# Kernel optimization log

Hardware: AMD Instinct MI355X
Metric: run time of the kernel (lower is better)

The kernel has to match this reference:

```python
import jax, jax.numpy as jnp
import numpy as np

EPS = 1e-08
RMAX = 8.0          # hist_range_max
BINS = 256
ALPHA = 0.02        # kalman_alpha (EMA rate)
THRESH = -2.0       # mask_threshold


def setup_inputs() -> dict:
    key = jax.random.key(0)
    B, C, L = 4, 5, 2097152
    x = jax.random.normal(key, (B, C, L), dtype=jnp.float32)
    # running histogram buffer, initialized to ones as in the module
    hist = jnp.ones((C, BINS), dtype=jnp.float32)
    # analytic reference log-pdfs over the bin grid
    grid = jnp.linspace(EPS, RMAX, BINS)
    logp_ref = jnp.stack([
        jnp.log(grid) - 0.5 * grid ** 2,                 # Rayleigh-like (A)
        -1.5 * jnp.log1p((grid / (RMAX / 2)) ** 2),      # heavy-tail (theta')
        -grid,                                            # exponential (A^2)
        -0.5 * grid ** 2,                                 # half-gaussian (AA')
        -0.5 * grid ** 2,                                 # half-gaussian (A^2 theta')
    ], axis=0) + EPS
    return {"x": x, "hist": hist, "logp_ref": logp_ref.astype(jnp.float32)}


def reference(x, hist, logp_ref):
    B, C, L = x.shape
    # NOTE: torch does x.reshape(C, -1) on a (B, C, L) tensor, i.e. a raw
    # memory reinterpretation (no permute). Replicate exactly.
    flat_abs = jnp.abs(x.reshape(C, B * L))                     # (C, B*L)
    # per-channel 99th-percentile normalization (linear interpolation, like torch)
    max_vals = jnp.maximum(
        jnp.quantile(flat_abs, 0.99, axis=-1, keepdims=True), EPS)
    normalized = flat_abs / max_vals * RMAX
    clipped = jnp.clip(normalized, 0.0, RMAX - EPS)
    idx = (clipped / RMAX * (BINS - 1)).astype(jnp.int32)       # floor (nonneg)
    idx = jnp.clip(idx, 0, BINS - 1)                            # (C, B*L)

    # histogram scatter-add per channel (vectorized over all channels)
    ch = jnp.broadcast_to(jnp.arange(C)[:, None], idx.shape)
    new_hist = jnp.zeros((C, BINS), dtype=x.dtype).at[ch, idx].add(1.0)

    # EMA update of the running histogram
    hist = (1.0 - ALPHA) * hist + ALPHA * new_hist
    smoothed = hist + EPS
    logp_obs = jnp.log(smoothed / jnp.sum(smoothed, axis=-1, keepdims=True))

    # gather per-sample log-probs and form the log-likelihood ratio
    logp_ref_s = jnp.take_along_axis(logp_ref, idx, axis=-1)   # (C, B*L)
    logp_obs_s = jnp.take_along_axis(logp_obs, idx, axis=-1)   # (C, B*L)
    Lam = (logp_ref_s - logp_obs_s).reshape(B, C, L)

    mask = jax.nn.sigmoid(-(Lam - THRESH))   # beta = 1.0
    return x * mask
```

## Files before the change

### kernel.cpp

```cpp
#include <hip/hip_runtime.h>
#include <math.h>

typedef unsigned int u32;
typedef unsigned long long u64;
typedef long long i64;

#define BINS 256
#define TBITS 0x40000000u
#define OOBBITS 0x42000000u
#define A_BASE 131072u
#define A_BINS 4096
#define B_BINS 8192
#define SLOT 2048
#define NBLK 512


__device__ __forceinline__ int bin_index_f32(float xv, float mv) {
    float r = __fdiv_rn(fabsf(xv), mv);
    r = fminf(r, 1.0f);
    return (int)__fmul_rn(r, 255.0f);
}

template<int PER>
__device__ void block_select(const u32* __restrict__ h, u32 target,
                             u32* ssum, u32* res) {
    const int t = threadIdx.x;
    u32 loc[PER];
    u32 s = 0;
    const int base = t * PER;
#pragma unroll
    for (int j = 0; j < PER; ++j) { loc[j] = h[base + j]; s += loc[j]; }
    ssum[t] = s;
    __syncthreads();
    for (int off = 1; off < 256; off <<= 1) {
        u32 add = (t >= off) ? ssum[t - off] : 0;
        __syncthreads();
        ssum[t] += add;
        __syncthreads();
    }
    u32 cum = ssum[t] - s;
#pragma unroll
    for (int j = 0; j < PER; ++j) {
        u32 cnt = loc[j];
        if (target >= cum && target < cum + cnt) { res[0] = (u32)(base + j); res[1] = target - cum; }
        cum += cnt;
    }
    __syncthreads();
}

__device__ __forceinline__ float np_lerp_f32(u32 v0bits, u32 v1bits, double gamma) {
    float v0 = __uint_as_float(v0bits);
    float v1 = __uint_as_float(v1bits);
    float dba = __fsub_rn(v1, v0);
    float q;
    if (gamma >= 0.5) q = __fsub_rn(v1, __fmul_rn(dba, (float)(1.0 - gamma)));
    else              q = __fadd_rn(v0, __fmul_rn(dba, (float)gamma));
    return fmaxf(q, 1e-8f);
}


__global__ __launch_bounds__(256) void k_pass1(const float* __restrict__ x, u32* __restrict__ cand,
                                               u32* __restrict__ oflow, i64 nper, int do_cand) {
    __shared__ u32 lbuf[SLOT];
    __shared__ u32 lcnt;
    const int c = blockIdx.y;
    if (threadIdx.x == 0) lcnt = 0;
    __syncthreads();
    const float* xc = x + (i64)c * nper;
    const i64 nv = nper >> 2;
    const float4* xv = (const float4*)xc;
    for (i64 i = (i64)blockIdx.x * 256 + threadIdx.x; i < nv; i += (i64)gridDim.x * 256) {
        float4 v = xv[i];
        u32 b;
        b = __float_as_uint(fabsf(v.x));
        if (b >= TBITS) { u32 p = atomicAdd(&lcnt, 1u); if (p < SLOT) lbuf[p] = b; }
        b = __float_as_uint(fabsf(v.y));
        if (b >= TBITS) { u32 p = atomicAdd(&lcnt, 1u); if (p < SLOT) lbuf[p] = b; }
        b = __float_as_uint(fabsf(v.z));
        if (b >= TBITS) { u32 p = atomicAdd(&lcnt, 1u); if (p < SLOT) lbuf[p] = b; }
        b = __float_as_uint(fabsf(v.w));
        if (b >= TBITS) { u32 p = atomicAdd(&lcnt, 1u); if (p < SLOT) lbuf[p] = b; }
    }
    if (blockIdx.x == 0 && threadIdx.x < (int)(nper & 3)) {
        u32 b = __float_as_uint(fabsf(xc[nv * 4 + threadIdx.x]));
        if (b >= TBITS) { u32 p = atomicAdd(&lcnt, 1u); if (p < SLOT) lbuf[p] = b; }
    }
    __syncthreads();
    if (threadIdx.x == 0 && lcnt > SLOT) {
        atomicExch(&oflow[c], 1u);
        lcnt = SLOT;
    }
    __syncthreads();
    if (do_cand) {
        const u32 cnt = lcnt;
        u32* slot = cand + ((i64)c * gridDim.x + blockIdx.x) * SLOT;
        for (u32 j = threadIdx.x; j < SLOT; j += 256)
            slot[j] = (j < cnt) ? lbuf[j] : 0u;
    }
}


__global__ __launch_bounds__(256) void k_cselA_hist(const u32* __restrict__ cand,
                                                    u32* __restrict__ gha, u32* __restrict__ goob, i64 ntot) {
    __shared__ u32 ha[A_BINS];
    __shared__ u32 loob;
    const int c = blockIdx.y;
    for (int i = threadIdx.x; i < A_BINS; i += 256) ha[i] = 0;
    if (threadIdx.x == 0) loob = 0;
    __syncthreads();
    const uint4* cd = (const uint4*)(cand + (i64)c * ntot);
    const i64 nv4 = ntot >> 2;
    for (i64 i = (i64)blockIdx.x * 256 + threadIdx.x; i < nv4; i += (i64)gridDim.x * 256) {
        uint4 v = cd[i];
        u32 b;
        b = v.x; if (b >= TBITS) { u32 bin = (b >> 13) - A_BASE; if (bin >= A_BINS) { atomicAdd(&loob, 1u); bin = A_BINS - 1; } atomicAdd(&ha[bin], 1u); }
        b = v.y; if (b >= TBITS) { u32 bin = (b >> 13) - A_BASE; if (bin >= A_BINS) { atomicAdd(&loob, 1u); bin = A_BINS - 1; } atomicAdd(&ha[bin], 1u); }
        b = v.z; if (b >= TBITS) { u32 bin = (b >> 13) - A_BASE; if (bin >= A_BINS) { atomicAdd(&loob, 1u); bin = A_BINS - 1; } atomicAdd(&ha[bin], 1u); }
        b = v.w; if (b >= TBITS) { u32 bin = (b >> 13) - A_BASE; if (bin >= A_BINS) { atomicAdd(&loob, 1u); bin = A_BINS - 1; } atomicAdd(&ha[bin], 1u); }
    }
    __syncthreads();
    for (int i = threadIdx.x; i < A_BINS; i += 256)
        if (ha[i]) atomicAdd(&gha[c * A_BINS + i], ha[i]);
    if (threadIdx.x == 0 && loob) atomicExch(&goob[c], 1u);
}

__global__ __launch_bounds__(256) void k_cselA_pick(const u32* __restrict__ gha,
                                                    const u32* __restrict__ oflow, const u32* __restrict__ goob,
                                                    u32* __restrict__ flag, u32* __restrict__ cselA, u32 needed) {
    __shared__ u32 ssum[256];
    __shared__ u32 pr[4];
    __shared__ u32 s_total;
    const int c = blockIdx.x;
    const int t = threadIdx.x;
    if (t < 4) pr[t] = 0;
    const u32* h = gha + c * A_BINS;
    u32 loc[16];
    u32 s = 0;
    const int base = t * 16;
#pragma unroll
    for (int j = 0; j < 16; ++j) { loc[j] = h[base + j]; s += loc[j]; }
    ssum[t] = s;
    __syncthreads();
    for (int off = 1; off < 256; off <<= 1) {
        u32 add = (t >= off) ? ssum[t - off] : 0;
        __syncthreads();
        ssum[t] += add;
        __syncthreads();
    }
    if (t == 255) s_total = ssum[255];
    __syncthreads();
    const u32 total = s_total;
    const u32 bad = (oflow[c] != 0) || (goob[c] != 0) || (total < needed) || (needed < 2);
    if (t == 0) flag[c] = bad;
    if (bad) return;
    const u32 t0 = total - needed;
    const u32 t1 = t0 + 1;
    u32 cum = ssum[t] - s;
#pragma unroll
    for (int j = 0; j < 16; ++j) {
        u32 cnt = loc[j];
        if (t0 >= cum && t0 < cum + cnt) { pr[0] = (u32)(base + j); pr[1] = t0 - cum; }
        if (t1 >= cum && t1 < cum + cnt) { pr[2] = (u32)(base + j); pr[3] = t1 - cum; }
        cum += cnt;
    }
    __syncthreads();
    if (t == 0) {
        cselA[c * 4 + 0] = pr[0]; cselA[c * 4 + 1] = pr[1];
        cselA[c * 4 + 2] = pr[2]; cselA[c * 4 + 3] = pr[3];
    }
}


__global__ __launch_bounds__(256) void k_cselB_hist(const u32* __restrict__ cand, const u32* __restrict__ flag,
                                                    const u32* __restrict__ cselA,
                                                    u32* __restrict__ g3a, u32* __restrict__ g3b, i64 ntot) {
    const int c = blockIdx.y;
    if (flag[c]) return;
    __shared__ u32 la[B_BINS], lb[B_BINS];
    for (int i = threadIdx.x; i < B_BINS; i += 256) { la[i] = 0; lb[i] = 0; }
    __syncthreads();
    const u32 topA0 = A_BASE + cselA[c * 4 + 0];
    const u32 topA1 = A_BASE + cselA[c * 4 + 2];
    const u32* cd = cand + (i64)c * ntot;
    for (i64 i = (i64)blockIdx.x * 256 + threadIdx.x; i < ntot; i += (i64)gridDim.x * 256) {
        u32 v = cd[i];
        if (v >= TBITS) {
            u32 tbin = v >> 13;
            if (tbin == topA0) atomicAdd(&la[v & (B_BINS - 1)], 1u);
            if (tbin == topA1) atomicAdd(&lb[v & (B_BINS - 1)], 1u);
        }
    }
    __syncthreads();
    for (int i = threadIdx.x; i < B_BINS; i += 256) {
        if (la[i]) atomicAdd(&g3a[c * B_BINS + i], la[i]);
        if (lb[i]) atomicAdd(&g3b[c * B_BINS + i], lb[i]);
    }
}

__global__ __launch_bounds__(256) void k_cselB_pick(const u32* __restrict__ g3a, const u32* __restrict__ g3b,
                                                    const u32* __restrict__ flag, const u32* __restrict__ cselA,
                                                    float* __restrict__ mv, double gamma) {
    __shared__ u32 ssum[256];
    __shared__ u32 pr[4];
    const int c = blockIdx.x;
    if (flag[c]) return;
    if (threadIdx.x < 4) pr[threadIdx.x] = 0;
    __syncthreads();
    block_select<32>(g3a + c * B_BINS, cselA[c * 4 + 1], ssum, &pr[0]);
    block_select<32>(g3b + c * B_BINS, cselA[c * 4 + 3], ssum, &pr[2]);
    if (threadIdx.x == 0) {
        u32 v0bits = ((A_BASE + cselA[c * 4 + 0]) << 13) | pr[0];
        u32 v1bits = ((A_BASE + cselA[c * 4 + 2]) << 13) | pr[2];
        mv[c] = np_lerp_f32(v0bits, v1bits, gamma);
    }
}

__global__ void k_flag_force(u32* __restrict__ flag, int C) {
    if (threadIdx.x < C) flag[threadIdx.x] = 1u;
}


__global__ __launch_bounds__(256) void k_fallback(const float* __restrict__ x, const u32* __restrict__ flag,
                                                  float* __restrict__ mv, i64 nper, u32 k0, double gamma) {
    const int c = blockIdx.x;
    if (!flag[c]) return;
    __shared__ u32 h0[2048], h1[2048];
    __shared__ u32 ssum[256];
    __shared__ u32 pr[4];
    __shared__ u32 st[4];
    const float* xc = x + (i64)c * nper;
    const i64 nv = nper >> 2;
    const int rem = (int)(nper & 3);
    const float4* xv = (const float4*)xc;
    const int t = threadIdx.x;

    for (int i = t; i < 1024; i += 256) h0[i] = 0;
    __syncthreads();
    for (i64 i = t; i < nv; i += 256) {
        float4 v = xv[i];
        atomicAdd(&h0[__float_as_uint(fabsf(v.x)) >> 21], 1u);
        atomicAdd(&h0[__float_as_uint(fabsf(v.y)) >> 21], 1u);
        atomicAdd(&h0[__float_as_uint(fabsf(v.z)) >> 21], 1u);
        atomicAdd(&h0[__float_as_uint(fabsf(v.w)) >> 21], 1u);
    }
    if (t < rem) atomicAdd(&h0[__float_as_uint(fabsf(xc[nv * 4 + t])) >> 21], 1u);
    __syncthreads();
    if (t < 4) pr[t] = 0;
    __syncthreads();
    block_select<4>(h0, k0, ssum, &pr[0]);
    block_select<4>(h0, k0 + 1, ssum, &pr[2]);
    if (t < 4) st[t] = pr[t];
    __syncthreads();

    const u32 p0 = st[0], p1 = st[2];
    for (int i = t; i < 2048; i += 256) { h0[i] = 0; h1[i] = 0; }
    __syncthreads();
    for (i64 i = t; i < nv; i += 256) {
        float4 v = xv[i];
        u32 b;
        b = __float_as_uint(fabsf(v.x));
        if ((b >> 21) == p0) atomicAdd(&h0[(b >> 10) & 2047], 1u);
        if ((b >> 21) == p1) atomicAdd(&h1[(b >> 10) & 2047], 1u);
        b = __float_as_uint(fabsf(v.y));
        if ((b >> 21) == p0) atomicAdd(&h0[(b >> 10) & 2047], 1u);
        if ((b >> 21) == p1) atomicAdd(&h1[(b >> 10) & 2047], 1u);
        b = __float_as_uint(fabsf(v.z));
        if ((b >> 21) == p0) atomicAdd(&h0[(b >> 10) & 2047], 1u);
        if ((b >> 21) == p1) atomicAdd(&h1[(b >> 10) & 2047], 1u);
        b = __float_as_uint(fabsf(v.w));
        if ((b >> 21) == p0) atomicAdd(&h0[(b >> 10) & 2047], 1u);
        if ((b >> 21) == p1) atomicAdd(&h1[(b >> 10) & 2047], 1u);
    }
    if (t < rem) {
        u32 b = __float_as_uint(fabsf(xc[nv * 4 + t]));
        if ((b >> 21) == p0) atomicAdd(&h0[(b >> 10) & 2047], 1u);
        if ((b >> 21) == p1) atomicAdd(&h1[(b >> 10) & 2047], 1u);
    }
    __syncthreads();
    if (t < 4) pr[t] = 0;
    __syncthreads();
    block_select<8>(h0, st[1], ssum, &pr[0]);
    block_select<8>(h1, st[3], ssum, &pr[2]);
    if (t == 0) { st[0] = (p0 << 11) | pr[0]; st[1] = pr[1]; st[2] = (p1 << 11) | pr[2]; st[3] = pr[3]; }
    __syncthreads();

    const u32 q0 = st[0], q1 = st[2];
    for (int i = t; i < 1024; i += 256) { h0[i] = 0; h1[i] = 0; }
    __syncthreads();
    for (i64 i = t; i < nv; i += 256) {
        float4 v = xv[i];
        u32 b;
        b = __float_as_uint(fabsf(v.x));
        if ((b >> 10) == q0) atomicAdd(&h0[b & 1023], 1u);
        if ((b >> 10) == q1) atomicAdd(&h1[b & 1023], 1u);
        b = __float_as_uint(fabsf(v.y));
        if ((b >> 10) == q0) atomicAdd(&h0[b & 1023], 1u);
        if ((b >> 10) == q1) atomicAdd(&h1[b & 1023], 1u);
        b = __float_as_uint(fabsf(v.z));
        if ((b >> 10) == q0) atomicAdd(&h0[b & 1023], 1u);
        if ((b >> 10) == q1) atomicAdd(&h1[b & 1023], 1u);
        b = __float_as_uint(fabsf(v.w));
        if ((b >> 10) == q0) atomicAdd(&h0[b & 1023], 1u);
        if ((b >> 10) == q1) atomicAdd(&h1[b & 1023], 1u);
    }
    if (t < rem) {
        u32 b = __float_as_uint(fabsf(xc[nv * 4 + t]));
        if ((b >> 10) == q0) atomicAdd(&h0[b & 1023], 1u);
        if ((b >> 10) == q1) atomicAdd(&h1[b & 1023], 1u);
    }
    __syncthreads();
    if (t < 4) pr[t] = 0;
    __syncthreads();
    block_select<4>(h0, st[1], ssum, &pr[0]);
    block_select<4>(h1, st[3], ssum, &pr[2]);
    if (t == 0) {
        u32 v0bits = (q0 << 10) | pr[0];
        u32 v1bits = (q1 << 10) | pr[2];
        mv[c] = np_lerp_f32(v0bits, v1bits, gamma);
    }
}


__global__ __launch_bounds__(256) void k_hist_idx(const float* __restrict__ x, const float* __restrict__ mv,
                                                  u32* __restrict__ h256, i64 nper) {
    __shared__ u32 lh[8][257];
    const int c = blockIdx.y;
    const float m = mv[c];
    for (int i = threadIdx.x; i < 8 * 257; i += 256) (&lh[0][0])[i] = 0;
    __syncthreads();
    const float* xc = x + (i64)c * nper;
    const i64 nv = nper >> 2;
    const int copy = threadIdx.x & 7;
    const float4* xv = (const float4*)xc;
    for (i64 i = (i64)blockIdx.x * 256 + threadIdx.x; i < nv; i += (i64)gridDim.x * 256) {
        float4 v = xv[i];
        atomicAdd(&lh[copy][bin_index_f32(v.x, m)], 1u);
        atomicAdd(&lh[copy][bin_index_f32(v.y, m)], 1u);
        atomicAdd(&lh[copy][bin_index_f32(v.z, m)], 1u);
        atomicAdd(&lh[copy][bin_index_f32(v.w, m)], 1u);
    }
    if (blockIdx.x == 0 && threadIdx.x < (int)(nper & 3)) {
        atomicAdd(&lh[copy][bin_index_f32(xc[nv * 4 + threadIdx.x], m)], 1u);
    }
    __syncthreads();
    for (int i = threadIdx.x; i < BINS; i += 256) {
        u32 s = 0;
#pragma unroll
        for (int k = 0; k < 8; ++k) s += lh[k][i];
        if (s) atomicAdd(&h256[c * BINS + i], s);
    }
}


__global__ void k_mask_table(const float* __restrict__ hist_in, const float* __restrict__ logp_ref,
                             const u32* __restrict__ h256, double* __restrict__ mask) {
    __shared__ double sm[BINS];
    __shared__ double ssum;
    const int c = blockIdx.x;
    const int b = threadIdx.x;
    float h = hist_in[c * BINS + b];
    float n = (float)h256[c * BINS + b];
    float t = __fadd_rn(__fmul_rn(0.98f, h), __fmul_rn(0.02f, n));
    float smf = __fadd_rn(t, 1e-8f);
    double smoothed = (double)smf;
    sm[b] = smoothed;
    __syncthreads();
    if (b == 0) { double s = 0.0; for (int i = 0; i < BINS; ++i) s += sm[i]; ssum = s; }
    __syncthreads();
    double logp_obs = log(smoothed / ssum);
    double Lam = (double)logp_ref[c * BINS + b] - logp_obs;
    mask[c * BINS + b] = 1.0 / (1.0 + exp(Lam + 2.0));
}


__global__ __launch_bounds__(256) void k_output(const float* __restrict__ x, const float* __restrict__ mv,
                                                const double* __restrict__ mask, float* __restrict__ out, i64 nper) {
    const int c = blockIdx.y;
    const float m = mv[c];
    const double* mt = mask + c * BINS;
    const float* xc = x + (i64)c * nper;
    float* oc = out + (i64)c * nper;
    const i64 nv = nper >> 2;
    const float4* xv = (const float4*)xc;
    float4* ov = (float4*)oc;
    for (i64 i = (i64)blockIdx.x * 256 + threadIdx.x; i < nv; i += (i64)gridDim.x * 256) {
        float4 v = xv[i];
        float4 o;
        o.x = (float)((double)v.x * mt[bin_index_f32(v.x, m)]);
        o.y = (float)((double)v.y * mt[bin_index_f32(v.y, m)]);
        o.z = (float)((double)v.z * mt[bin_index_f32(v.z, m)]);
        o.w = (float)((double)v.w * mt[bin_index_f32(v.w, m)]);
        ov[i] = o;
    }
    if (blockIdx.x == 0 && threadIdx.x < (int)(nper & 3)) {
        i64 i = nv * 4 + threadIdx.x;
        float v = xc[i];
        oc[i] = (float)((double)v * mt[bin_index_f32(v, m)]);
    }
}


extern "C" void kernel_launch(void* const* d_in, const int* in_sizes, int n_in,
                              void* d_out, int out_size, void* d_ws, size_t ws_size,
                              hipStream_t stream) {
    const float* x        = (const float*)d_in[0];
    const float* hist_in  = (const float*)d_in[1];
    const float* logp_ref = (const float*)d_in[2];
    float* out = (float*)d_out;

    const int C = in_sizes[1] / BINS;
    const i64 total = (i64)in_sizes[0];
    const i64 nper = total / C;

    char* w = (char*)d_ws;
    size_t off = 0;
    float*  mv   = (float*)(w + off);  off += 4 * ((C + 7) & ~7);
    double* mask = (double*)(w + off); off += 8 * BINS * C;
    u32* h256   = (u32*)(w + off); off += 4 * BINS * C;
    u32* oflow  = (u32*)(w + off); off += 4 * C;
    u32* goob   = (u32*)(w + off); off += 4 * C;
    u32* flag   = (u32*)(w + off); off += 4 * C;
    u32* cselA  = (u32*)(w + off); off += 4 * 4 * C;
    u32* gha    = (u32*)(w + off); off += 4 * A_BINS * C;
    u32* g3a    = (u32*)(w + off); off += 4 * B_BINS * C;
    u32* g3b    = (u32*)(w + off); off += 4 * B_BINS * C;
    const size_t zbytes = off;
    off = (off + 255) & ~(size_t)255;
    u32* cand = (u32*)(w + off);
    const i64 ntot = (i64)NBLK * SLOT;
    const size_t cand_bytes = (size_t)4 * (size_t)C * (size_t)ntot;
    const int do_cand = (ws_size >= off + cand_bytes) ? 1 : 0;

    hipMemsetAsync(d_ws, 0, zbytes, stream);

    const double virt = 0.99 * (double)(nper - 1);
    const i64 k0 = (i64)floor(virt);
    const double gamma = virt - (double)k0;
    const u32 needed = (u32)(nper - k0);

    dim3 blk(256);
    dim3 grd(NBLK, (unsigned)C);
    dim3 grd64(64, (unsigned)C);

    k_pass1<<<grd, blk, 0, stream>>>(x, cand, oflow, nper, do_cand);
    if (do_cand) {
        k_cselA_hist<<<grd64, blk, 0, stream>>>(cand, gha, goob, ntot);
        k_cselA_pick<<<(unsigned)C, blk, 0, stream>>>(gha, oflow, goob, flag, cselA, needed);
        k_cselB_hist<<<grd64, blk, 0, stream>>>(cand, flag, cselA, g3a, g3b, ntot);
        k_cselB_pick<<<(unsigned)C, blk, 0, stream>>>(g3a, g3b, flag, cselA, mv, gamma);
    } else {
        k_flag_force<<<1, 64, 0, stream>>>(flag, C);
    }
    k_fallback<<<(unsigned)C, blk, 0, stream>>>(x, flag, mv, nper, (u32)k0, gamma);
    k_hist_idx<<<grd, blk, 0, stream>>>(x, mv, h256, nper);
    k_mask_table<<<(unsigned)C, BINS, 0, stream>>>(hist_in, logp_ref, h256, mask);
    k_output<<<grd, blk, 0, stream>>>(x, mv, mask, out, nper);
}
```

Baseline: 207.7 us.

## Fuse coarse histogram into pass1 and mask table into output kernel

Builds the coarse A histogram inside the first pass over x, which removes the separate kernel that re-read the candidate buffer. The mask table is now computed per block in shared memory at the start of the output kernel, so one launch and the global double-table lookups go away. Main loops now process two float4 per iteration, and the candidate slot size shrinks to cut candidate buffer traffic. In exchange each output block redundantly recomputes 256 log/exp values, pass1 needs more shared memory per block, and the smaller slot makes overflow into the fallback path more likely.

```diff
diff --git a/kernel.cpp b/kernel.cpp
--- a/kernel.cpp
+++ b/kernel.cpp
@@ -7,11 +7,10 @@
 
 #define BINS 256
 #define TBITS 0x40000000u
-#define OOBBITS 0x42000000u
 #define A_BASE 131072u
 #define A_BINS 4096
 #define B_BINS 8192
-#define SLOT 2048
+#define SLOT 1536
 #define NBLK 512
 
 
@@ -60,35 +59,52 @@
 
 
 __global__ __launch_bounds__(256) void k_pass1(const float* __restrict__ x, u32* __restrict__ cand,
-                                               u32* __restrict__ oflow, i64 nper, int do_cand) {
+                                               u32* __restrict__ gha, u32* __restrict__ oflow,
+                                               u32* __restrict__ goob, i64 nper, int do_cand) {
     __shared__ u32 lbuf[SLOT];
-    __shared__ u32 lcnt;
+    __shared__ u32 lha[A_BINS];
+    __shared__ u32 lcnt, loob;
     const int c = blockIdx.y;
-    if (threadIdx.x == 0) lcnt = 0;
+    for (int i = threadIdx.x; i < A_BINS; i += 256) lha[i] = 0;
+    if (threadIdx.x == 0) { lcnt = 0; loob = 0; }
     __syncthreads();
     const float* xc = x + (i64)c * nper;
-    const i64 nv = nper >> 2;
+    const i64 nv2 = nper >> 3;
     const float4* xv = (const float4*)xc;
-    for (i64 i = (i64)blockIdx.x * 256 + threadIdx.x; i < nv; i += (i64)gridDim.x * 256) {
-        float4 v = xv[i];
-        u32 b;
-        b = __float_as_uint(fabsf(v.x));
-        if (b >= TBITS) { u32 p = atomicAdd(&lcnt, 1u); if (p < SLOT) lbuf[p] = b; }
-        b = __float_as_uint(fabsf(v.y));
-        if (b >= TBITS) { u32 p = atomicAdd(&lcnt, 1u); if (p < SLOT) lbuf[p] = b; }
-        b = __float_as_uint(fabsf(v.z));
-        if (b >= TBITS) { u32 p = atomicAdd(&lcnt, 1u); if (p < SLOT) lbuf[p] = b; }
-        b = __float_as_uint(fabsf(v.w));
-        if (b >= TBITS) { u32 p = atomicAdd(&lcnt, 1u); if (p < SLOT) lbuf[p] = b; }
-    }
-    if (blockIdx.x == 0 && threadIdx.x < (int)(nper & 3)) {
-        u32 b = __float_as_uint(fabsf(xc[nv * 4 + threadIdx.x]));
-        if (b >= TBITS) { u32 p = atomicAdd(&lcnt, 1u); if (p < SLOT) lbuf[p] = b; }
-    }
-    __syncthreads();
-    if (threadIdx.x == 0 && lcnt > SLOT) {
-        atomicExch(&oflow[c], 1u);
-        lcnt = SLOT;
+    for (i64 i = (i64)blockIdx.x * 256 + threadIdx.x; i < nv2; i += (i64)gridDim.x * 256) {
+        float4 a = xv[2 * i], b = xv[2 * i + 1];
+        u32 bb[8];
+        bb[0] = __float_as_uint(fabsf(a.x)); bb[1] = __float_as_uint(fabsf(a.y));
+        bb[2] = __float_as_uint(fabsf(a.z)); bb[3] = __float_as_uint(fabsf(a.w));
+        bb[4] = __float_as_uint(fabsf(b.x)); bb[5] = __float_as_uint(fabsf(b.y));
+        bb[6] = __float_as_uint(fabsf(b.z)); bb[7] = __float_as_uint(fabsf(b.w));
+#pragma unroll
+        for (int k = 0; k < 8; ++k) {
+            if (bb[k] >= TBITS) {
+                u32 p = atomicAdd(&lcnt, 1u);
+                if (p < SLOT) lbuf[p] = bb[k];
+                u32 bin = (bb[k] >> 13) - A_BASE;
+                if (bin >= A_BINS) { atomicAdd(&loob, 1u); bin = A_BINS - 1; }
+                atomicAdd(&lha[bin], 1u);
+            }
+        }
+    }
+    if (blockIdx.x == 0 && threadIdx.x < (int)(nper & 7)) {
+        u32 b = __float_as_uint(fabsf(xc[nv2 * 8 + threadIdx.x]));
+        if (b >= TBITS) {
+            u32 p = atomicAdd(&lcnt, 1u);
+            if (p < SLOT) lbuf[p] = b;
+            u32 bin = (b >> 13) - A_BASE;
+            if (bin >= A_BINS) { atomicAdd(&loob, 1u); bin = A_BINS - 1; }
+            atomicAdd(&lha[bin], 1u);
+        }
+    }
+    __syncthreads();
+    for (int i = threadIdx.x; i < A_BINS; i += 256)
+        if (lha[i]) atomicAdd(&gha[c * A_BINS + i], lha[i]);
+    if (threadIdx.x == 0) {
+        if (loob) atomicExch(&goob[c], 1u);
+        if (lcnt > SLOT) { atomicExch(&oflow[c], 1u); lcnt = SLOT; }
     }
     __syncthreads();
     if (do_cand) {
@@ -99,30 +115,6 @@
     }
 }
 
-
-__global__ __launch_bounds__(256) void k_cselA_hist(const u32* __restrict__ cand,
-                                                    u32* __restrict__ gha, u32* __restrict__ goob, i64 ntot) {
-    __shared__ u32 ha[A_BINS];
-    __shared__ u32 loob;
-    const int c = blockIdx.y;
-    for (int i = threadIdx.x; i < A_BINS; i += 256) ha[i] = 0;
-    if (threadIdx.x == 0) loob = 0;
-    __syncthreads();
-    const uint4* cd = (const uint4*)(cand + (i64)c * ntot);
-    const i64 nv4 = ntot >> 2;
-    for (i64 i = (i64)blockIdx.x * 256 + threadIdx.x; i < nv4; i += (i64)gridDim.x * 256) {
-        uint4 v = cd[i];
-        u32 b;
-        b = v.x; if (b >= TBITS) { u32 bin = (b >> 13) - A_BASE; if (bin >= A_BINS) { atomicAdd(&loob, 1u); bin = A_BINS - 1; } atomicAdd(&ha[bin], 1u); }
-        b = v.y; if (b >= TBITS) { u32 bin = (b >> 13) - A_BASE; if (bin >= A_BINS) { atomicAdd(&loob, 1u); bin = A_BINS - 1; } atomicAdd(&ha[bin], 1u); }
-        b = v.z; if (b >= TBITS) { u32 bin = (b >> 13) - A_BASE; if (bin >= A_BINS) { atomicAdd(&loob, 1u); bin = A_BINS - 1; } atomicAdd(&ha[bin], 1u); }
-        b = v.w; if (b >= TBITS) { u32 bin = (b >> 13) - A_BASE; if (bin >= A_BINS) { atomicAdd(&loob, 1u); bin = A_BINS - 1; } atomicAdd(&ha[bin], 1u); }
-    }
-    __syncthreads();
-    for (int i = threadIdx.x; i < A_BINS; i += 256)
-        if (ha[i]) atomicAdd(&gha[c * A_BINS + i], ha[i]);
-    if (threadIdx.x == 0 && loob) atomicExch(&goob[c], 1u);
-}
 
 __global__ __launch_bounds__(256) void k_cselA_pick(const u32* __restrict__ gha,
                                                     const u32* __restrict__ oflow, const u32* __restrict__ goob,
@@ -181,14 +173,19 @@
     __syncthreads();
     const u32 topA0 = A_BASE + cselA[c * 4 + 0];
     const u32 topA1 = A_BASE + cselA[c * 4 + 2];
-    const u32* cd = cand + (i64)c * ntot;
-    for (i64 i = (i64)blockIdx.x * 256 + threadIdx.x; i < ntot; i += (i64)gridDim.x * 256) {
-        u32 v = cd[i];
-        if (v >= TBITS) {
-            u32 tbin = v >> 13;
-            if (tbin == topA0) atomicAdd(&la[v & (B_BINS - 1)], 1u);
-            if (tbin == topA1) atomicAdd(&lb[v & (B_BINS - 1)], 1u);
-        }
+    const uint4* cd = (const uint4*)(cand + (i64)c * ntot);
+    const i64 nv4 = ntot >> 2;
+    for (i64 i = (i64)blockIdx.x * 256 + threadIdx.x; i < nv4; i += (i64)gridDim.x * 256) {
+        uint4 v = cd[i];
+        u32 b;
+        b = v.x;
+        if (b >= TBITS) { u32 tb = b >> 13; if (tb == topA0) atomicAdd(&la[b & (B_BINS - 1)], 1u); if (tb == topA1) atomicAdd(&lb[b & (B_BINS - 1)], 1u); }
+        b = v.y;
+        if (b >= TBITS) { u32 tb = b >> 13; if (tb == topA0) atomicAdd(&la[b & (B_BINS - 1)], 1u); if (tb == topA1) atomicAdd(&lb[b & (B_BINS - 1)], 1u); }
+        b = v.z;
+        if (b >= TBITS) { u32 tb = b >> 13; if (tb == topA0) atomicAdd(&la[b & (B_BINS - 1)], 1u); if (tb == topA1) atomicAdd(&lb[b & (B_BINS - 1)], 1u); }
+        b = v.w;
+        if (b >= TBITS) { u32 tb = b >> 13; if (tb == topA0) atomicAdd(&la[b & (B_BINS - 1)], 1u); if (tb == topA1) atomicAdd(&lb[b & (B_BINS - 1)], 1u); }
     }
     __syncthreads();
     for (int i = threadIdx.x; i < B_BINS; i += 256) {
@@ -329,18 +326,22 @@
     for (int i = threadIdx.x; i < 8 * 257; i += 256) (&lh[0][0])[i] = 0;
     __syncthreads();
     const float* xc = x + (i64)c * nper;
-    const i64 nv = nper >> 2;
+    const i64 nv2 = nper >> 3;
     const int copy = threadIdx.x & 7;
     const float4* xv = (const float4*)xc;
-    for (i64 i = (i64)blockIdx.x * 256 + threadIdx.x; i < nv; i += (i64)gridDim.x * 256) {
-        float4 v = xv[i];
-        atomicAdd(&lh[copy][bin_index_f32(v.x, m)], 1u);
-        atomicAdd(&lh[copy][bin_index_f32(v.y, m)], 1u);
-        atomicAdd(&lh[copy][bin_index_f32(v.z, m)], 1u);
-        atomicAdd(&lh[copy][bin_index_f32(v.w, m)], 1u);
-    }
-    if (blockIdx.x == 0 && threadIdx.x < (int)(nper & 3)) {
-        atomicAdd(&lh[copy][bin_index_f32(xc[nv * 4 + threadIdx.x], m)], 1u);
+    for (i64 i = (i64)blockIdx.x * 256 + threadIdx.x; i < nv2; i += (i64)gridDim.x * 256) {
+        float4 a = xv[2 * i], b = xv[2 * i + 1];
+        atomicAdd(&lh[copy][bin_index_f32(a.x, m)], 1u);
+        atomicAdd(&lh[copy][bin_index_f32(a.y, m)], 1u);
+        atomicAdd(&lh[copy][bin_index_f32(a.z, m)], 1u);
+        atomicAdd(&lh[copy][bin_index_f32(a.w, m)], 1u);
+        atomicAdd(&lh[copy][bin_index_f32(b.x, m)], 1u);
+        atomicAdd(&lh[copy][bin_index_f32(b.y, m)], 1u);
+        atomicAdd(&lh[copy][bin_index_f32(b.z, m)], 1u);
+        atomicAdd(&lh[copy][bin_index_f32(b.w, m)], 1u);
+    }
+    if (blockIdx.x == 0 && threadIdx.x < (int)(nper & 7)) {
+        atomicAdd(&lh[copy][bin_index_f32(xc[nv2 * 8 + threadIdx.x], m)], 1u);
     }
     __syncthreads();
     for (int i = threadIdx.x; i < BINS; i += 256) {
@@ -352,50 +353,55 @@
 }
 
 
-__global__ void k_mask_table(const float* __restrict__ hist_in, const float* __restrict__ logp_ref,
-                             const u32* __restrict__ h256, double* __restrict__ mask) {
-    __shared__ double sm[BINS];
-    __shared__ double ssum;
-    const int c = blockIdx.x;
+__global__ __launch_bounds__(256) void k_output(const float* __restrict__ x, const float* __restrict__ mv,
+                                                const float* __restrict__ hist_in, const float* __restrict__ logp_ref,
+                                                const u32* __restrict__ h256, float* __restrict__ out, i64 nper) {
+    __shared__ double smv_s[BINS];
+    __shared__ double maskl[BINS];
+    __shared__ double stot;
+    const int c = blockIdx.y;
     const int b = threadIdx.x;
     float h = hist_in[c * BINS + b];
-    float n = (float)h256[c * BINS + b];
-    float t = __fadd_rn(__fmul_rn(0.98f, h), __fmul_rn(0.02f, n));
+    float nn = (float)h256[c * BINS + b];
+    float t = __fadd_rn(__fmul_rn(0.98f, h), __fmul_rn(0.02f, nn));
     float smf = __fadd_rn(t, 1e-8f);
-    double smoothed = (double)smf;
-    sm[b] = smoothed;
-    __syncthreads();
-    if (b == 0) { double s = 0.0; for (int i = 0; i < BINS; ++i) s += sm[i]; ssum = s; }
-    __syncthreads();
-    double logp_obs = log(smoothed / ssum);
-    double Lam = (double)logp_ref[c * BINS + b] - logp_obs;
-    mask[c * BINS + b] = 1.0 / (1.0 + exp(Lam + 2.0));
-}
-
-
-__global__ __launch_bounds__(256) void k_output(const float* __restrict__ x, const float* __restrict__ mv,
-                                                const double* __restrict__ mask, float* __restrict__ out, i64 nper) {
-    const int c = blockIdx.y;
+    double sm = (double)smf;
+    smv_s[b] = sm;
+    __syncthreads();
+    if (b < 64) {
+        double s = smv_s[b] + smv_s[b + 64] + smv_s[b + 128] + smv_s[b + 192];
+        for (int o = 32; o; o >>= 1) s += __shfl_down(s, o);
+        if (b == 0) stot = s;
+    }
+    __syncthreads();
+    double Lam = (double)logp_ref[c * BINS + b] - log(sm / stot);
+    maskl[b] = 1.0 / (1.0 + exp(Lam + 2.0));
+    __syncthreads();
+
     const float m = mv[c];
-    const double* mt = mask + c * BINS;
     const float* xc = x + (i64)c * nper;
     float* oc = out + (i64)c * nper;
-    const i64 nv = nper >> 2;
+    const i64 nv2 = nper >> 3;
     const float4* xv = (const float4*)xc;
     float4* ov = (float4*)oc;
-    for (i64 i = (i64)blockIdx.x * 256 + threadIdx.x; i < nv; i += (i64)gridDim.x * 256) {
-        float4 v = xv[i];
-        float4 o;
-        o.x = (float)((double)v.x * mt[bin_index_f32(v.x, m)]);
-        o.y = (float)((double)v.y * mt[bin_index_f32(v.y, m)]);
-        o.z = (float)((double)v.z * mt[bin_index_f32(v.z, m)]);
-        o.w = (float)((double)v.w * mt[bin_index_f32(v.w, m)]);
-        ov[i] = o;
-    }
-    if (blockIdx.x == 0 && threadIdx.x < (int)(nper & 3)) {
-        i64 i = nv * 4 + threadIdx.x;
+    for (i64 i = (i64)blockIdx.x * 256 + threadIdx.x; i < nv2; i += (i64)gridDim.x * 256) {
+        float4 a = xv[2 * i], bb = xv[2 * i + 1];
+        float4 oa, ob;
+        oa.x = (float)((double)a.x * maskl[bin_index_f32(a.x, m)]);
+        oa.y = (float)((double)a.y * maskl[bin_index_f32(a.y, m)]);
+        oa.z = (float)((double)a.z * maskl[bin_index_f32(a.z, m)]);
+        oa.w = (float)((double)a.w * maskl[bin_index_f32(a.w, m)]);
+        ob.x = (float)((double)bb.x * maskl[bin_index_f32(bb.x, m)]);
+        ob.y = (float)((double)bb.y * maskl[bin_index_f32(bb.y, m)]);
+        ob.z = (float)((double)bb.z * maskl[bin_index_f32(bb.z, m)]);
+        ob.w = (float)((double)bb.w * maskl[bin_index_f32(bb.w, m)]);
+        ov[2 * i] = oa;
+        ov[2 * i + 1] = ob;
+    }
+    if (blockIdx.x == 0 && threadIdx.x < (int)(nper & 7)) {
+        i64 i = nv2 * 8 + threadIdx.x;
         float v = xc[i];
-        oc[i] = (float)((double)v * mt[bin_index_f32(v, m)]);
+        oc[i] = (float)((double)v * maskl[bin_index_f32(v, m)]);
     }
 }
 
@@ -415,7 +421,6 @@
     char* w = (char*)d_ws;
     size_t off = 0;
     float*  mv   = (float*)(w + off);  off += 4 * ((C + 7) & ~7);
-    double* mask = (double*)(w + off); off += 8 * BINS * C;
     u32* h256   = (u32*)(w + off); off += 4 * BINS * C;
     u32* oflow  = (u32*)(w + off); off += 4 * C;
     u32* goob   = (u32*)(w + off); off += 4 * C;
@@ -442,9 +447,8 @@
     dim3 grd(NBLK, (unsigned)C);
     dim3 grd64(64, (unsigned)C);
 
-    k_pass1<<<grd, blk, 0, stream>>>(x, cand, oflow, nper, do_cand);
+    k_pass1<<<grd, blk, 0, stream>>>(x, cand, gha, oflow, goob, nper, do_cand);
     if (do_cand) {
-        k_cselA_hist<<<grd64, blk, 0, stream>>>(cand, gha, goob, ntot);
         k_cselA_pick<<<(unsigned)C, blk, 0, stream>>>(gha, oflow, goob, flag, cselA, needed);
         k_cselB_hist<<<grd64, blk, 0, stream>>>(cand, flag, cselA, g3a, g3b, ntot);
         k_cselB_pick<<<(unsigned)C, blk, 0, stream>>>(g3a, g3b, flag, cselA, mv, gamma);
@@ -453,6 +457,5 @@
     }
     k_fallback<<<(unsigned)C, blk, 0, stream>>>(x, flag, mv, nper, (u32)k0, gamma);
     k_hist_idx<<<grd, blk, 0, stream>>>(x, mv, h256, nper);
-    k_mask_table<<<(unsigned)C, BINS, 0, stream>>>(hist_in, logp_ref, h256, mask);
-    k_output<<<grd, blk, 0, stream>>>(x, mv, mask, out, nper);
-}
+    k_output<<<grd, blk, 0, stream>>>(x, mv, hist_in, logp_ref, h256, out, nper);
+}
```

New measurement: 194.9 us. -6.2%, faster.
